# Performance work log

Measured on AMD Instinct MI355X. Metric: run time of the kernel, lower is better.

Reference implementation:

```python
import jax, jax.numpy as jnp
import numpy as np
from jax import lax

EPS = 1e-5
WBITS, BBITS, ABITS = 8, 8, 11  # weight/bias/activation precisions (class defaults)


def _ste_round(x):
    # straight-through estimator round (matches HAWQ-style fake quant)
    return x + lax.stop_gradient(jnp.round(x) - x)


def _quant_weight(w, bits):
    # symmetric per-output-channel weight quantization
    n = 2.0 ** (bits - 1) - 1.0
    s = lax.stop_gradient(jnp.max(jnp.abs(w.reshape(w.shape[0], -1)), axis=1)) / n
    s = jnp.maximum(s, 1e-8)
    w_int = jnp.clip(_ste_round(w / s[:, None, None, None]), -n - 1.0, n)
    return w_int, s


def _conv(x, w, stride, pad):
    return lax.conv_general_dilated(
        x, w, (stride, stride), ((pad, pad), (pad, pad)),
        dimension_numbers=('NCHW', 'OIHW', 'NCHW'))


def _quant_bn_conv(x, act_scale, w, gamma, beta, mean, var, stride, pad):
    # fold BN into conv (QuantBnConv2d), quantize folded weight per channel,
    # integer conv in the x/act_scale domain, rescale back to float
    f = gamma * lax.rsqrt(var + EPS)
    w_f = w * f[:, None, None, None]
    b_f = beta - mean * f
    w_int, w_s = _quant_weight(w_f, WBITS)
    nb = 2.0 ** (BBITS - 1) - 1.0
    b_s = w_s * act_scale  # [O]
    b_int = jnp.clip(_ste_round(b_f / b_s), -nb - 1.0, nb)
    x_int = x / act_scale
    y_int = _conv(x_int, w_int, stride, pad) + b_int[None, :, None, None]
    return y_int * b_s[None, :, None, None], w_s


def _quant_conv(x, act_scale, w, stride, pad):
    # plain QuantConv2d (shortcut path, no bias)
    w_int, w_s = _quant_weight(w, WBITS)
    y_int = _conv(x / act_scale, w_int, stride, pad)
    scale = w_s * act_scale  # [O]
    return y_int * scale[None, :, None, None], w_s


def _quant_act(x, bits):
    # QuantAct: symmetric dynamic requantization to `bits` bits
    n = 2.0 ** (bits - 1) - 1.0
    s = jnp.maximum(lax.stop_gradient(jnp.max(jnp.abs(x))) / n, 1e-8)
    xq = jnp.clip(_ste_round(x / s), -n - 1.0, n) * s
    return xq, s


def setup_inputs() -> dict:
    key = jax.random.key(0)
    ks = jax.random.split(key, 12)
    B, Cin, Cout, H = 64, 128, 256, 56
    return {
        'x': jax.random.normal(ks[0], (B, Cin, H, H), jnp.float32),
        'act_scale': jnp.ones((1,), jnp.float32) * 0.05,
        'w_sc': jax.random.normal(ks[1], (Cout, Cin, 1, 1), jnp.float32) * 0.05,
        'w1': jax.random.normal(ks[2], (Cout, Cin, 3, 3), jnp.float32) * 0.05,
        'g1': jax.random.uniform(ks[3], (Cout,), jnp.float32) + 0.5,
        'b1': jax.random.normal(ks[4], (Cout,), jnp.float32) * 0.1,
        'm1': jax.random.normal(ks[5], (Cout,), jnp.float32) * 0.1,
        'v1': jax.random.uniform(ks[6], (Cout,), jnp.float32) + 0.5,
        'w2': jax.random.normal(ks[7], (Cout, Cout, 3, 3), jnp.float32) * 0.05,
        'g2': jax.random.uniform(ks[8], (Cout,), jnp.float32) + 0.5,
        'b2': jax.random.normal(ks[9], (Cout,), jnp.float32) * 0.1,
        'm2': jax.random.normal(ks[10], (Cout,), jnp.float32) * 0.1,
        'v2': jax.random.uniform(ks[11], (Cout,), jnp.float32) + 0.5,
    }


def reference(x, act_scale, w_sc, w1, g1, b1, m1, v1, w2, g2, b2, m2, v2):
    # resize_identity branch of QBlock.forward (stride-2 stage transition)
    short_x, _ = _quant_conv(x, act_scale, w_sc, stride=2, pad=0)
    out, _ = _quant_bn_conv(x, act_scale, w1, g1, b1, m1, v1, stride=2, pad=1)
    out = jax.nn.relu(out)
    out, a = _quant_act(out, ABITS)
    out, _ = _quant_bn_conv(out, a, w2, g2, b2, m2, v2, stride=1, pad=1)
    out = jax.nn.relu(out)
    out, a = _quant_act(out, ABITS)
    out = jax.nn.relu(out + short_x)
    out, a = _quant_act(out, ABITS)
    return out, a
```

## Files before the change

kernel.cpp:

```cpp
#include <hip/hip_runtime.h>
#include <cstdio>
#include <cstdint>

typedef _Float16 h8 __attribute__((ext_vector_type(8)));
typedef _Float16 h4 __attribute__((ext_vector_type(4)));
typedef _Float16 h2 __attribute__((ext_vector_type(2)));
typedef float f4 __attribute__((ext_vector_type(4)));

#define GLD16(g, l) __builtin_amdgcn_global_load_lds( \
    (const __attribute__((address_space(1))) void*)(g), \
    (__attribute__((address_space(3))) void*)(l), 16, 0, 0)

static constexpr int HOUT = 28;
static constexpr long long NSP = 64LL * HOUT * HOUT;
static constexpr long long NEL = NSP * 256;
static constexpr int NSLOT = 64;
static constexpr int SLOTSTRIDE = 32;

__global__ void init_ws(int* __restrict__ slots, _Float16* __restrict__ zp)
{
    const int t = threadIdx.x;
    for (int i = t; i < 3 * NSLOT * SLOTSTRIDE; i += 256) slots[i] = 0;
    for (int i = t; i < 512; i += 256) zp[i] = (_Float16)0.f;
}

__device__ __forceinline__ float slot_max(const int* __restrict__ slots)
{
    float m = 0.f;
#pragma unroll
    for (int i = 0; i < NSLOT; ++i) m = fmaxf(m, __int_as_float(slots[i * SLOTSTRIDE]));
    return m;
}

__global__ void prep_w1(const float* __restrict__ w1, const float* __restrict__ g1,
                        const float* __restrict__ b1, const float* __restrict__ m1,
                        const float* __restrict__ v1, const float* __restrict__ asp,
                        _Float16* __restrict__ wq, float* __restrict__ scale1,
                        float* __restrict__ bias1)
{
    const int o = blockIdx.x, t = threadIdx.x;
    const float f = g1[o] * rsqrtf(v1[o] + 1e-5f);
    const float* wr = w1 + (size_t)o * 1152;
    float amax = 0.f;
    for (int i = t; i < 1152; i += 256) amax = fmaxf(amax, fabsf(wr[i] * f));
    __shared__ float red[256];
    red[t] = amax; __syncthreads();
    for (int s = 128; s > 0; s >>= 1) { if (t < s) red[t] = fmaxf(red[t], red[t + s]); __syncthreads(); }
    const float ws = fmaxf(red[0] / 127.f, 1e-8f);
    for (int idx = t; idx < 2304; idx += 256) {
        int p = idx >> 8, cc = idx & 255, ci = cc & 127;
        float q = fminf(fmaxf(rintf(wr[ci * 9 + p] * f / ws), -128.f), 127.f);
        wq[(size_t)o * 2304 + idx] = (_Float16)q;
    }
    if (t == 0) {
        const float bs = ws * asp[0];
        const float bf = b1[o] - m1[o] * f;
        float bq = fminf(fmaxf(rintf(bf / bs), -128.f), 127.f);
        scale1[o] = bs;
        bias1[o] = bq * bs;
    }
}

__global__ void prep_w2(const float* __restrict__ w2, const float* __restrict__ g2,
                        const float* __restrict__ b2, const float* __restrict__ m2,
                        const float* __restrict__ v2,
                        _Float16* __restrict__ wq, float* __restrict__ ws2,
                        float* __restrict__ b2f)
{
    const int o = blockIdx.x, t = threadIdx.x;
    const float f = g2[o] * rsqrtf(v2[o] + 1e-5f);
    const float* wr = w2 + (size_t)o * 2304;
    float amax = 0.f;
    for (int i = t; i < 2304; i += 256) amax = fmaxf(amax, fabsf(wr[i] * f));
    __shared__ float red[256];
    red[t] = amax; __syncthreads();
    for (int s = 128; s > 0; s >>= 1) { if (t < s) red[t] = fmaxf(red[t], red[t + s]); __syncthreads(); }
    const float ws = fmaxf(red[0] / 127.f, 1e-8f);
    for (int idx = t; idx < 2304; idx += 256) {
        int p = idx >> 8, ci = idx & 255;
        float q = fminf(fmaxf(rintf(wr[ci * 9 + p] * f / ws), -128.f), 127.f);
        wq[(size_t)o * 2304 + idx] = (_Float16)q;
    }
    if (t == 0) { ws2[o] = ws; b2f[o] = b2[o] - m2[o] * f; }
}

__global__ void prep_wsc(const float* __restrict__ wsc, const float* __restrict__ asp,
                         _Float16* __restrict__ wq, float* __restrict__ scale_sc)
{
    const int o = blockIdx.x, t = threadIdx.x;
    const float* wr = wsc + (size_t)o * 128;
    float amax = (t < 128) ? fabsf(wr[t]) : 0.f;
    __shared__ float red[256];
    red[t] = amax; __syncthreads();
    for (int s = 128; s > 0; s >>= 1) { if (t < s) red[t] = fmaxf(red[t], red[t + s]); __syncthreads(); }
    const float ws = fmaxf(red[0] / 127.f, 1e-8f);
    float q = fminf(fmaxf(rintf(wr[t & 127] / ws), -128.f), 127.f);
    wq[(size_t)o * 256 + t] = (_Float16)q;
    if (t == 0) scale_sc[o] = ws * asp[0];
}

__global__ void prep_x(const float* __restrict__ x, const float* __restrict__ asp,
                       _Float16* __restrict__ xf)
{
    const int b = blockIdx.x / 56, h = blockIdx.x - (blockIdx.x / 56) * 56;
    const float as = asp[0];
    __shared__ float tile[56 * 129];
    const float* src = x + ((size_t)b * 128 * 56 + h) * 56;
    for (int i = threadIdx.x; i < 7168; i += 256) {
        int c = i / 56, ww = i - c * 56;
        tile[ww * 129 + c] = src[(size_t)c * 3136 + ww] / as;
    }
    __syncthreads();
    _Float16* dst = xf + (size_t)(b * 56 + h) * 56 * 256;
    for (int j = threadIdx.x; j < 7168; j += 256) {
        int ww = j >> 7, q = j & 127;
        int cc = q * 2;
        int c0 = cc & 127, c1 = (cc + 1) & 127;
        float x0 = tile[ww * 129 + c0];
        float x1 = tile[ww * 129 + c1];
        h2 o;
        if (cc < 128) { o[0] = (_Float16)x0; o[1] = (_Float16)x1; }
        else {
            _Float16 h0 = (_Float16)x0, h1 = (_Float16)x1;
            o[0] = (_Float16)(x0 - (float)h0);
            o[1] = (_Float16)(x1 - (float)h1);
        }
        *(h2*)&dst[(size_t)j * 2] = o;
    }
}

template<int HINP, int WINP, int STRIDE, bool SC>
__global__ __launch_bounds__(256, 2)
void conv_k(const _Float16* __restrict__ Xf,
            const _Float16* __restrict__ Wq,
            const _Float16* __restrict__ Wsc,
            const float* __restrict__ scale,
            const float* __restrict__ bias,
            const float* __restrict__ scale_sc,
            float* __restrict__ Y,
            float* __restrict__ Ysc,
            int* __restrict__ slots,
            const _Float16* __restrict__ zp)
{
    constexpr int KT = 2304;
    __shared__ __attribute__((aligned(16))) _Float16 As[4096];
    __shared__ __attribute__((aligned(16))) _Float16 Bs[4096];
    __shared__ float wred[4];

    const int t = threadIdx.x;
    const int wave = t >> 6, lane = t & 63;
    const int wm = wave >> 1, wn = wave & 1;
    const int fr = lane & 15, fq = lane >> 4;
    const int m0 = blockIdx.y << 7;
    const int n0 = blockIdx.x << 7;
    const int chunk = t & 3;
    const int rowt = t >> 2;

    int bb[2], oh[2], ow[2];
#pragma unroll
    for (int i = 0; i < 2; ++i) {
        int n = n0 + i * 64 + rowt;
        bb[i] = n / (HOUT * HOUT);
        int r = n - bb[i] * (HOUT * HOUT);
        oh[i] = r / HOUT;
        ow[i] = r - oh[i] * HOUT;
    }

    const char* Ab = (const char*)Wq + ((size_t)m0 * KT + (size_t)chunk * 8) * 2;
    size_t aoff[2];
#pragma unroll
    for (int i = 0; i < 2; ++i) aoff[i] = (size_t)(i * 64 + rowt) * (KT * 2);

    f4 acc[4][4];
    f4 accs[4][4];
#pragma unroll
    for (int i = 0; i < 4; ++i)
#pragma unroll
        for (int j = 0; j < 4; ++j) {
            acc[i][j] = f4{0.f, 0.f, 0.f, 0.f};
            if constexpr (SC) accs[i][j] = f4{0.f, 0.f, 0.f, 0.f};
        }

#pragma unroll 1
    for (int p = 0; p < 9; ++p) {
        const int kh = p / 3, kw = p - kh * 3;
        const char* bsrc[2];
#pragma unroll
        for (int i = 0; i < 2; ++i) {
            int ih = oh[i] * STRIDE - 1 + kh;
            int iw = ow[i] * STRIDE - 1 + kw;
            bool ok = ((unsigned)ih < (unsigned)HINP) && ((unsigned)iw < (unsigned)WINP);
            bsrc[i] = ok ? (const char*)Xf + ((((size_t)bb[i] * HINP + ih) * WINP + iw) * 256 + (size_t)chunk * 8) * 2
                         : (const char*)zp + (size_t)chunk * 16;
        }
        const char* ap = Ab + (size_t)p * 512;
#pragma unroll 1
        for (int kc = 0; kc < 8; ++kc) {
#pragma unroll
            for (int i = 0; i < 2; ++i) {
                GLD16(ap + aoff[i] + kc * 64, (char*)As + i * 4096 + wave * 1024);
                GLD16(bsrc[i] + kc * 64,      (char*)Bs + i * 4096 + wave * 1024);
            }
            __syncthreads();
            h8 af[4], bf[4];
#pragma unroll
            for (int x = 0; x < 4; ++x) {
                af[x] = *(const h8*)&As[(wm * 64 + x * 16 + fr) * 32 + fq * 8];
                bf[x] = *(const h8*)&Bs[(wn * 64 + x * 16 + fr) * 32 + fq * 8];
            }
#pragma unroll
            for (int mi = 0; mi < 4; ++mi)
#pragma unroll
                for (int ni = 0; ni < 4; ++ni)
                    acc[mi][ni] = __builtin_amdgcn_mfma_f32_16x16x32_f16(af[mi], bf[ni], acc[mi][ni], 0, 0, 0);
            if constexpr (SC) {
                if (p == 4) {
                    h8 sf[4];
#pragma unroll
                    for (int mi = 0; mi < 4; ++mi)
                        sf[mi] = *(const h8*)&Wsc[(size_t)(m0 + wm * 64 + mi * 16 + fr) * 256 + kc * 32 + fq * 8];
#pragma unroll
                    for (int mi = 0; mi < 4; ++mi)
#pragma unroll
                        for (int ni = 0; ni < 4; ++ni)
                            accs[mi][ni] = __builtin_amdgcn_mfma_f32_16x16x32_f16(sf[mi], bf[ni], accs[mi][ni], 0, 0, 0);
                }
            }
            __syncthreads();
        }
    }

    float tmax = 0.f;
#pragma unroll
    for (int mi = 0; mi < 4; ++mi) {
        const int m = m0 + wm * 64 + mi * 16 + fq * 4;
        const f4 sc = *(const f4*)&scale[m];
        const f4 bi = *(const f4*)&bias[m];
        f4 ssc;
        if constexpr (SC) ssc = *(const f4*)&scale_sc[m];
#pragma unroll
        for (int ni = 0; ni < 4; ++ni) {
            const int n = n0 + wn * 64 + ni * 16 + fr;
            f4 v = acc[mi][ni] * sc + bi;
            f4 r;
            r.x = fmaxf(v.x, 0.f); r.y = fmaxf(v.y, 0.f);
            r.z = fmaxf(v.z, 0.f); r.w = fmaxf(v.w, 0.f);
            tmax = fmaxf(tmax, fmaxf(fmaxf(r.x, r.y), fmaxf(r.z, r.w)));
            *(f4*)&Y[(size_t)n * 256 + m] = r;
            if constexpr (SC) {
                f4 s = accs[mi][ni] * ssc;
                *(f4*)&Ysc[(size_t)n * 256 + m] = s;
            }
        }
    }
#pragma unroll
    for (int off = 32; off > 0; off >>= 1)
        tmax = fmaxf(tmax, __shfl_xor(tmax, off));
    if (lane == 0) wred[wave] = tmax;
    __syncthreads();
    if (t == 0) {
        float mx = fmaxf(fmaxf(wred[0], wred[1]), fmaxf(wred[2], wred[3]));
        atomicMax(&slots[((blockIdx.x + blockIdx.y * 392) & (NSLOT - 1)) * SLOTSTRIDE],
                  __float_as_int(mx));
    }
}

__global__ void mid_k(const int* __restrict__ slotsA, const float* __restrict__ ws2,
                      const float* __restrict__ b2f, float* __restrict__ scale2,
                      float* __restrict__ bias2, float* __restrict__ a1p)
{
    const int o = threadIdx.x;
    const float a1 = fmaxf(slot_max(slotsA) / 1023.f, 1e-8f);
    const float s2 = ws2[o] * a1;
    float bq = fminf(fmaxf(rintf(b2f[o] / s2), -128.f), 127.f);
    scale2[o] = s2;
    bias2[o] = bq * s2;
    if (o == 0) a1p[0] = a1;
}

__global__ void quant_x2(const float* __restrict__ t1, const float* __restrict__ a1p,
                         _Float16* __restrict__ x2)
{
    const size_t i = (size_t)blockIdx.x * 256 + threadIdx.x;
    const float a1 = a1p[0];
    f4 v = ((const f4*)t1)[i];
    h4 o;
    o[0] = (_Float16)fminf(rintf(v.x / a1), 1023.f);
    o[1] = (_Float16)fminf(rintf(v.y / a1), 1023.f);
    o[2] = (_Float16)fminf(rintf(v.z / a1), 1023.f);
    o[3] = (_Float16)fminf(rintf(v.w / a1), 1023.f);
    ((h4*)x2)[i] = o;
}

__global__ void add_short_k(const float* __restrict__ t2, const float* __restrict__ sh,
                            const int* __restrict__ slotsB, int* __restrict__ slotsC,
                            float* __restrict__ o3)
{
    const float a2 = fmaxf(slot_max(slotsB) / 1023.f, 1e-8f);
    const float inv_a2 = 1.f / a2;
    float tmax = 0.f;
    const size_t base = (size_t)blockIdx.x * 256 + threadIdx.x;
#pragma unroll
    for (int it = 0; it < 4; ++it) {
        const size_t i = base + (size_t)it * 802816;
        f4 v = ((const f4*)t2)[i];
        f4 s = ((const f4*)sh)[i];
        f4 r;
        r.x = fmaxf(fminf(rintf(v.x * inv_a2), 1023.f) * a2 + s.x, 0.f);
        r.y = fmaxf(fminf(rintf(v.y * inv_a2), 1023.f) * a2 + s.y, 0.f);
        r.z = fmaxf(fminf(rintf(v.z * inv_a2), 1023.f) * a2 + s.z, 0.f);
        r.w = fmaxf(fminf(rintf(v.w * inv_a2), 1023.f) * a2 + s.w, 0.f);
        ((f4*)o3)[i] = r;
        tmax = fmaxf(tmax, fmaxf(fmaxf(r.x, r.y), fmaxf(r.z, r.w)));
    }
#pragma unroll
    for (int off = 32; off > 0; off >>= 1)
        tmax = fmaxf(tmax, __shfl_xor(tmax, off));
    __shared__ float wred[4];
    if ((threadIdx.x & 63) == 0) wred[threadIdx.x >> 6] = tmax;
    __syncthreads();
    if (threadIdx.x == 0) {
        float mx = fmaxf(fmaxf(wred[0], wred[1]), fmaxf(wred[2], wred[3]));
        atomicMax(&slotsC[(blockIdx.x & (NSLOT - 1)) * SLOTSTRIDE], __float_as_int(mx));
    }
}

__global__ void finalize_k(const float* __restrict__ o3, const int* __restrict__ slotsC,
                           float* __restrict__ dout, int out_size)
{
    const int b = blockIdx.x / 28, oh = blockIdx.x - (blockIdx.x / 28) * 28;
    const float a3 = fmaxf(slot_max(slotsC) / 1023.f, 1e-8f);
    __shared__ float tile[28 * 257];
    const float* src = o3 + (size_t)(b * 28 + oh) * 28 * 256;
    for (int i = threadIdx.x; i < 7168; i += 256)
        tile[(i >> 8) * 257 + (i & 255)] = src[i];
    __syncthreads();
    for (int j = threadIdx.x; j < 7168; j += 256) {
        int c = j / 28, ww = j - (j / 28) * 28;
        float v = tile[ww * 257 + c];
        float q = fminf(rintf(v / a3), 1023.f);
        dout[(((size_t)b * 256 + c) * 28 + oh) * 28 + ww] = q * a3;
    }
    if (blockIdx.x == 0 && threadIdx.x == 0) dout[(size_t)out_size - 1] = a3;
}

extern "C" void kernel_launch(void* const* d_in, const int* in_sizes, int n_in,
                              void* d_out, int out_size, void* d_ws, size_t ws_size,
                              hipStream_t stream)
{
    const float* x   = (const float*)d_in[0];
    const float* as_ = (const float*)d_in[1];
    const float* wsc = (const float*)d_in[2];
    const float* w1  = (const float*)d_in[3];
    const float* g1  = (const float*)d_in[4];
    const float* b1  = (const float*)d_in[5];
    const float* m1  = (const float*)d_in[6];
    const float* v1  = (const float*)d_in[7];
    const float* w2  = (const float*)d_in[8];
    const float* g2  = (const float*)d_in[9];
    const float* b2  = (const float*)d_in[10];
    const float* m2  = (const float*)d_in[11];
    const float* v2  = (const float*)d_in[12];
    float* out = (float*)d_out;

    char* w = (char*)d_ws;
    size_t off = 0;
    auto alloc = [&](size_t bytes) { size_t c = off; off += (bytes + 255) & ~(size_t)255; return c; };
    const size_t oXF = alloc((size_t)64 * 56 * 56 * 256 * 2);
    const size_t oY1 = alloc((size_t)NEL * 4);
    const size_t oSH = alloc((size_t)NEL * 4);
    const size_t oX2 = alloc((size_t)NEL * 2);
    const size_t oW1 = alloc((size_t)256 * 2304 * 2);
    const size_t oW2 = alloc((size_t)256 * 2304 * 2);
    const size_t oWS = alloc((size_t)256 * 256 * 2);
    const size_t oSC = alloc((size_t)8 * 256 * 4);
    const size_t oMS = alloc(3 * NSLOT * SLOTSTRIDE * 4 + 2048);
    if (off > ws_size) {
        fprintf(stderr, "kernel_launch: ws too small: need %zu have %zu\n", off, ws_size);
        return;
    }

    _Float16* xf   = (_Float16*)(w + oXF);
    float*    y1   = (float*)(w + oY1);
    float*    sh   = (float*)(w + oSH);
    _Float16* x2   = (_Float16*)(w + oX2);
    _Float16* wq1  = (_Float16*)(w + oW1);
    _Float16* wq2  = (_Float16*)(w + oW2);
    _Float16* wscd = (_Float16*)(w + oWS);
    float* scl = (float*)(w + oSC);
    float *scale1 = scl, *bias1 = scl + 256, *scale_sc = scl + 512, *ws2 = scl + 768,
          *b2f = scl + 1024, *scale2 = scl + 1280, *bias2 = scl + 1536, *a1p = scl + 1792;
    int* slots  = (int*)(w + oMS);
    int* slotsA = slots;
    int* slotsB = slots + NSLOT * SLOTSTRIDE;
    int* slotsC = slots + 2 * NSLOT * SLOTSTRIDE;
    _Float16* zp = (_Float16*)(w + oMS + 3 * NSLOT * SLOTSTRIDE * 4);
    float* y2 = (float*)(w + oXF);
    float* o3 = (float*)(w + oY1);

    init_ws<<<1, 256, 0, stream>>>(slots, zp);
    prep_wsc<<<256, 256, 0, stream>>>(wsc, as_, wscd, scale_sc);
    prep_w1<<<256, 256, 0, stream>>>(w1, g1, b1, m1, v1, as_, wq1, scale1, bias1);
    prep_w2<<<256, 256, 0, stream>>>(w2, g2, b2, m2, v2, wq2, ws2, b2f);
    prep_x<<<64 * 56, 256, 0, stream>>>(x, as_, xf);
    conv_k<56, 56, 2, true><<<dim3(392, 2), 256, 0, stream>>>(
        xf, wq1, wscd, scale1, bias1, scale_sc, y1, sh, slotsA, zp);
    mid_k<<<1, 256, 0, stream>>>(slotsA, ws2, b2f, scale2, bias2, a1p);
    quant_x2<<<12544, 256, 0, stream>>>(y1, a1p, x2);
    conv_k<28, 28, 1, false><<<dim3(392, 2), 256, 0, stream>>>(
        x2, wq2, nullptr, scale2, bias2, nullptr, y2, nullptr, slotsB, zp);
    add_short_k<<<3136, 256, 0, stream>>>(y2, sh, slotsB, slotsC, o3);
    finalize_k<<<64 * 28, 256, 0, stream>>>(o3, slotsC, out, out_size);
}
```

Baseline: 362.3 us.

## Double-buffer conv GEMM loads, split shortcut conv, parity-split input layout

Rewrites the implicit-GEMM conv kernel to double-buffer its LDS tiles. The next k-step's global-to-LDS loads are issued before the current MFMAs, using explicit vmcnt waits and raw barriers. The stride-2 input is stored with even and odd columns split apart, giving contiguous gathers, and the shortcut 1x1 conv becomes its own kernel launch instead of being fused into the first conv. The block index is also swizzled and occupancy is raised to 3 blocks per SM. The cost is double the LDS and an extra launch that rereads the input for the shortcut.

```diff
diff --git a/kernel.cpp b/kernel.cpp
--- a/kernel.cpp
+++ b/kernel.cpp
@@ -111,7 +111,7 @@
         tile[ww * 129 + c] = src[(size_t)c * 3136 + ww] / as;
     }
     __syncthreads();
-    _Float16* dst = xf + (size_t)(b * 56 + h) * 56 * 256;
+    _Float16* dst = xf + (size_t)(b * 56 + h) * 2 * 28 * 256;
     for (int j = threadIdx.x; j < 7168; j += 256) {
         int ww = j >> 7, q = j & 127;
         int cc = q * 2;
@@ -125,143 +125,171 @@
             o[0] = (_Float16)(x0 - (float)h0);
             o[1] = (_Float16)(x1 - (float)h1);
         }
-        *(h2*)&dst[(size_t)j * 2] = o;
-    }
-}
-
-template<int HINP, int WINP, int STRIDE, bool SC>
-__global__ __launch_bounds__(256, 2)
+        size_t eo = ((size_t)(ww & 1) * 28 + (ww >> 1)) * 256 + (size_t)cc;
+        *(h2*)&dst[eo] = o;
+    }
+}
+
+template<int MODE>
+__global__ __launch_bounds__(256, 3)
 void conv_k(const _Float16* __restrict__ Xf,
             const _Float16* __restrict__ Wq,
-            const _Float16* __restrict__ Wsc,
             const float* __restrict__ scale,
             const float* __restrict__ bias,
-            const float* __restrict__ scale_sc,
             float* __restrict__ Y,
-            float* __restrict__ Ysc,
             int* __restrict__ slots,
             const _Float16* __restrict__ zp)
 {
-    constexpr int KT = 2304;
-    __shared__ __attribute__((aligned(16))) _Float16 As[4096];
-    __shared__ __attribute__((aligned(16))) _Float16 Bs[4096];
+    constexpr int KT = (MODE == 2) ? 256 : 2304;
+    constexpr int NSTEP = KT / 32;
+    __shared__ __attribute__((aligned(16))) _Float16 As[2][4096];
+    __shared__ __attribute__((aligned(16))) _Float16 Bs[2][4096];
     __shared__ float wred[4];
 
     const int t = threadIdx.x;
     const int wave = t >> 6, lane = t & 63;
     const int wm = wave >> 1, wn = wave & 1;
     const int fr = lane & 15, fq = lane >> 4;
-    const int m0 = blockIdx.y << 7;
-    const int n0 = blockIdx.x << 7;
-    const int chunk = t & 3;
-    const int rowt = t >> 2;
+
+    const int id = blockIdx.x;
+    const int lin = (id & 7) * 98 + (id >> 3);
+    const int m0 = (lin & 1) << 7;
+    const int n0 = (lin >> 1) << 7;
+
+    const int row_d = ((t >> 6) << 4) | (t & 15);
+    const int ch_d  = (t >> 4) & 3;
+
+    const char* aA[2];
+#pragma unroll
+    for (int i = 0; i < 2; ++i)
+        aA[i] = (const char*)Wq + (size_t)(m0 + i * 64 + row_d) * (KT * 2) + ch_d * 16;
 
     int bb[2], oh[2], ow[2];
+    const char* bC[2] = {nullptr, nullptr};
 #pragma unroll
     for (int i = 0; i < 2; ++i) {
-        int n = n0 + i * 64 + rowt;
-        bb[i] = n / (HOUT * HOUT);
-        int r = n - bb[i] * (HOUT * HOUT);
-        oh[i] = r / HOUT;
-        ow[i] = r - oh[i] * HOUT;
-    }
-
-    const char* Ab = (const char*)Wq + ((size_t)m0 * KT + (size_t)chunk * 8) * 2;
-    size_t aoff[2];
-#pragma unroll
-    for (int i = 0; i < 2; ++i) aoff[i] = (size_t)(i * 64 + rowt) * (KT * 2);
+        int n = n0 + i * 64 + row_d;
+        bb[i] = n / 784;
+        int r = n - bb[i] * 784;
+        oh[i] = r / 28;
+        ow[i] = r - oh[i] * 28;
+        if constexpr (MODE == 2)
+            bC[i] = (const char*)Xf +
+                ((((size_t)bb[i] * 56 + oh[i] * 2) * 2 + 0) * 28 + ow[i]) * 512 + ch_d * 16;
+    }
+
+    int aoffr[4], boffr[4];
+#pragma unroll
+    for (int x = 0; x < 4; ++x) {
+        aoffr[x] = wm * 4096 + (x * 64 + fq * 16 + fr) * 16;
+        boffr[x] = wn * 4096 + (x * 64 + fq * 16 + fr) * 16;
+    }
+
+    auto stage = [&](int ks, int buf) {
+        const int kc = ks & 7;
+#pragma unroll
+        for (int i = 0; i < 2; ++i)
+            GLD16(aA[i] + (size_t)ks * 64,
+                  (char*)As + buf * 8192 + i * 4096 + wave * 1024);
+        const int p = ks >> 3;
+        const int kh = p / 3, kw = p - kh * 3;
+#pragma unroll
+        for (int i = 0; i < 2; ++i) {
+            const char* bp;
+            if constexpr (MODE == 2) {
+                bp = bC[i] + ks * 64;
+            } else if constexpr (MODE == 0) {
+                int ih = oh[i] * 2 - 1 + kh;
+                int par = (kw == 1) ? 0 : 1;
+                int j = (kw == 0) ? ow[i] - 1 : ow[i];
+                bool ok = ((unsigned)ih < 56u) && ((unsigned)j < 28u);
+                bp = ok ? (const char*)Xf +
+                          (((((size_t)bb[i] * 56 + ih) * 2 + par) * 28 + j) << 9) + kc * 64 + ch_d * 16
+                        : (const char*)zp + ch_d * 16;
+            } else {
+                int ih = oh[i] - 1 + kh;
+                int iw = ow[i] - 1 + kw;
+                bool ok = ((unsigned)ih < 28u) && ((unsigned)iw < 28u);
+                bp = ok ? (const char*)Xf +
+                          ((((size_t)bb[i] * 28 + ih) * 28 + iw) << 9) + kc * 64 + ch_d * 16
+                        : (const char*)zp + ch_d * 16;
+            }
+            GLD16(bp, (char*)Bs + buf * 8192 + i * 4096 + wave * 1024);
+        }
+    };
 
     f4 acc[4][4];
-    f4 accs[4][4];
 #pragma unroll
     for (int i = 0; i < 4; ++i)
 #pragma unroll
-        for (int j = 0; j < 4; ++j) {
-            acc[i][j] = f4{0.f, 0.f, 0.f, 0.f};
-            if constexpr (SC) accs[i][j] = f4{0.f, 0.f, 0.f, 0.f};
-        }
-
+        for (int j = 0; j < 4; ++j) acc[i][j] = f4{0.f, 0.f, 0.f, 0.f};
+
+    stage(0, 0);
 #pragma unroll 1
-    for (int p = 0; p < 9; ++p) {
-        const int kh = p / 3, kw = p - kh * 3;
-        const char* bsrc[2];
-#pragma unroll
-        for (int i = 0; i < 2; ++i) {
-            int ih = oh[i] * STRIDE - 1 + kh;
-            int iw = ow[i] * STRIDE - 1 + kw;
-            bool ok = ((unsigned)ih < (unsigned)HINP) && ((unsigned)iw < (unsigned)WINP);
-            bsrc[i] = ok ? (const char*)Xf + ((((size_t)bb[i] * HINP + ih) * WINP + iw) * 256 + (size_t)chunk * 8) * 2
-                         : (const char*)zp + (size_t)chunk * 16;
-        }
-        const char* ap = Ab + (size_t)p * 512;
-#pragma unroll 1
-        for (int kc = 0; kc < 8; ++kc) {
-#pragma unroll
-            for (int i = 0; i < 2; ++i) {
-                GLD16(ap + aoff[i] + kc * 64, (char*)As + i * 4096 + wave * 1024);
-                GLD16(bsrc[i] + kc * 64,      (char*)Bs + i * 4096 + wave * 1024);
+    for (int ks = 0; ks < NSTEP; ++ks) {
+        const int cur = ks & 1;
+        if (ks + 1 < NSTEP) {
+            stage(ks + 1, cur ^ 1);
+            asm volatile("s_waitcnt vmcnt(4)" ::: "memory");
+        } else {
+            asm volatile("s_waitcnt vmcnt(0)" ::: "memory");
+        }
+        __builtin_amdgcn_s_barrier();
+        asm volatile("" ::: "memory");
+        h8 af[4], bf[4];
+#pragma unroll
+        for (int x = 0; x < 4; ++x) {
+            af[x] = *(const h8*)((const char*)As + cur * 8192 + aoffr[x]);
+            bf[x] = *(const h8*)((const char*)Bs + cur * 8192 + boffr[x]);
+        }
+#pragma unroll
+        for (int mi = 0; mi < 4; ++mi)
+#pragma unroll
+            for (int ni = 0; ni < 4; ++ni)
+                acc[mi][ni] = __builtin_amdgcn_mfma_f32_16x16x32_f16(af[mi], bf[ni], acc[mi][ni], 0, 0, 0);
+        asm volatile("" ::: "memory");
+        __builtin_amdgcn_s_barrier();
+    }
+
+    if constexpr (MODE == 2) {
+#pragma unroll
+        for (int mi = 0; mi < 4; ++mi) {
+            const int m = m0 + wm * 64 + mi * 16 + fq * 4;
+            const f4 sc = *(const f4*)&scale[m];
+#pragma unroll
+            for (int ni = 0; ni < 4; ++ni) {
+                const int n = n0 + wn * 64 + ni * 16 + fr;
+                f4 s = acc[mi][ni] * sc;
+                *(f4*)&Y[(size_t)n * 256 + m] = s;
             }
-            __syncthreads();
-            h8 af[4], bf[4];
-#pragma unroll
-            for (int x = 0; x < 4; ++x) {
-                af[x] = *(const h8*)&As[(wm * 64 + x * 16 + fr) * 32 + fq * 8];
-                bf[x] = *(const h8*)&Bs[(wn * 64 + x * 16 + fr) * 32 + fq * 8];
+        }
+    } else {
+        float tmax = 0.f;
+#pragma unroll
+        for (int mi = 0; mi < 4; ++mi) {
+            const int m = m0 + wm * 64 + mi * 16 + fq * 4;
+            const f4 sc = *(const f4*)&scale[m];
+            const f4 bi = *(const f4*)&bias[m];
+#pragma unroll
+            for (int ni = 0; ni < 4; ++ni) {
+                const int n = n0 + wn * 64 + ni * 16 + fr;
+                f4 v = acc[mi][ni] * sc + bi;
+                f4 r;
+                r.x = fmaxf(v.x, 0.f); r.y = fmaxf(v.y, 0.f);
+                r.z = fmaxf(v.z, 0.f); r.w = fmaxf(v.w, 0.f);
+                tmax = fmaxf(tmax, fmaxf(fmaxf(r.x, r.y), fmaxf(r.z, r.w)));
+                *(f4*)&Y[(size_t)n * 256 + m] = r;
             }
-#pragma unroll
-            for (int mi = 0; mi < 4; ++mi)
-#pragma unroll
-                for (int ni = 0; ni < 4; ++ni)
-                    acc[mi][ni] = __builtin_amdgcn_mfma_f32_16x16x32_f16(af[mi], bf[ni], acc[mi][ni], 0, 0, 0);
-            if constexpr (SC) {
-                if (p == 4) {
-                    h8 sf[4];
-#pragma unroll
-                    for (int mi = 0; mi < 4; ++mi)
-                        sf[mi] = *(const h8*)&Wsc[(size_t)(m0 + wm * 64 + mi * 16 + fr) * 256 + kc * 32 + fq * 8];
-#pragma unroll
-                    for (int mi = 0; mi < 4; ++mi)
-#pragma unroll
-                        for (int ni = 0; ni < 4; ++ni)
-                            accs[mi][ni] = __builtin_amdgcn_mfma_f32_16x16x32_f16(sf[mi], bf[ni], accs[mi][ni], 0, 0, 0);
-                }
-            }
-            __syncthreads();
-        }
-    }
-
-    float tmax = 0.f;
-#pragma unroll
-    for (int mi = 0; mi < 4; ++mi) {
-        const int m = m0 + wm * 64 + mi * 16 + fq * 4;
-        const f4 sc = *(const f4*)&scale[m];
-        const f4 bi = *(const f4*)&bias[m];
-        f4 ssc;
-        if constexpr (SC) ssc = *(const f4*)&scale_sc[m];
-#pragma unroll
-        for (int ni = 0; ni < 4; ++ni) {
-            const int n = n0 + wn * 64 + ni * 16 + fr;
-            f4 v = acc[mi][ni] * sc + bi;
-            f4 r;
-            r.x = fmaxf(v.x, 0.f); r.y = fmaxf(v.y, 0.f);
-            r.z = fmaxf(v.z, 0.f); r.w = fmaxf(v.w, 0.f);
-            tmax = fmaxf(tmax, fmaxf(fmaxf(r.x, r.y), fmaxf(r.z, r.w)));
-            *(f4*)&Y[(size_t)n * 256 + m] = r;
-            if constexpr (SC) {
-                f4 s = accs[mi][ni] * ssc;
-                *(f4*)&Ysc[(size_t)n * 256 + m] = s;
-            }
-        }
-    }
-#pragma unroll
-    for (int off = 32; off > 0; off >>= 1)
-        tmax = fmaxf(tmax, __shfl_xor(tmax, off));
-    if (lane == 0) wred[wave] = tmax;
-    __syncthreads();
-    if (t == 0) {
-        float mx = fmaxf(fmaxf(wred[0], wred[1]), fmaxf(wred[2], wred[3]));
-        atomicMax(&slots[((blockIdx.x + blockIdx.y * 392) & (NSLOT - 1)) * SLOTSTRIDE],
-                  __float_as_int(mx));
+        }
+#pragma unroll
+        for (int off = 32; off > 0; off >>= 1)
+            tmax = fmaxf(tmax, __shfl_xor(tmax, off));
+        if (lane == 0) wred[wave] = tmax;
+        __syncthreads();
+        if (t == 0) {
+            float mx = fmaxf(fmaxf(wred[0], wred[1]), fmaxf(wred[2], wred[3]));
+            atomicMax(&slots[(lin & (NSLOT - 1)) * SLOTSTRIDE], __float_as_int(mx));
+        }
     }
 }
 
@@ -403,12 +431,11 @@
     prep_w1<<<256, 256, 0, stream>>>(w1, g1, b1, m1, v1, as_, wq1, scale1, bias1);
     prep_w2<<<256, 256, 0, stream>>>(w2, g2, b2, m2, v2, wq2, ws2, b2f);
     prep_x<<<64 * 56, 256, 0, stream>>>(x, as_, xf);
-    conv_k<56, 56, 2, true><<<dim3(392, 2), 256, 0, stream>>>(
-        xf, wq1, wscd, scale1, bias1, scale_sc, y1, sh, slotsA, zp);
+    conv_k<2><<<784, 256, 0, stream>>>(xf, wscd, scale_sc, nullptr, sh, nullptr, zp);
+    conv_k<0><<<784, 256, 0, stream>>>(xf, wq1, scale1, bias1, y1, slotsA, zp);
     mid_k<<<1, 256, 0, stream>>>(slotsA, ws2, b2f, scale2, bias2, a1p);
     quant_x2<<<12544, 256, 0, stream>>>(y1, a1p, x2);
-    conv_k<28, 28, 1, false><<<dim3(392, 2), 256, 0, stream>>>(
-        x2, wq2, nullptr, scale2, bias2, nullptr, y2, nullptr, slotsB, zp);
+    conv_k<1><<<784, 256, 0, stream>>>(x2, wq2, scale2, bias2, y2, slotsB, zp);
     add_short_k<<<3136, 256, 0, stream>>>(y2, sh, slotsB, slotsC, o3);
     finalize_k<<<64 * 28, 256, 0, stream>>>(o3, slotsC, out, out_size);
 }
```

Measured after the change: 455.2 us. 25.6% more time.

## Restructure implicit-GEMM conv with 256x256 tiles and triple-buffered async LDS pipeline

Applied to the files above, without the earlier changes.

The conv kernel now uses 512-thread workgroups, each computing all 256 output channels for 256 spatial positions. It runs a 3-stage global_load_lds ring with vmcnt waits and one barrier per step, replacing the two-barrier single-buffer loop, and raises MFMA priority via setprio. The workgroup-to-XCD mapping is remapped, and prep_x writes x with even/odd width columns split so stride-2 gathers become contiguous. The 1x1 shortcut GEMM moves into a separate epilogue that reads straight from global memory. The aim is to hide load latency and reuse each weight load across more positions, at the cost of one workgroup per CU with a 96KB LDS footprint and only 196 workgroups.

```diff
diff --git a/kernel.cpp b/kernel.cpp
--- a/kernel.cpp
+++ b/kernel.cpp
@@ -111,7 +111,7 @@
         tile[ww * 129 + c] = src[(size_t)c * 3136 + ww] / as;
     }
     __syncthreads();
-    _Float16* dst = xf + (size_t)(b * 56 + h) * 56 * 256;
+    _Float16* dst = xf + (size_t)(b * 56 + h) * 2 * 28 * 256;
     for (int j = threadIdx.x; j < 7168; j += 256) {
         int ww = j >> 7, q = j & 127;
         int cc = q * 2;
@@ -125,12 +125,13 @@
             o[0] = (_Float16)(x0 - (float)h0);
             o[1] = (_Float16)(x1 - (float)h1);
         }
-        *(h2*)&dst[(size_t)j * 2] = o;
-    }
-}
-
-template<int HINP, int WINP, int STRIDE, bool SC>
-__global__ __launch_bounds__(256, 2)
+        size_t eo = ((size_t)(ww & 1) * 28 + (ww >> 1)) * 256 + (size_t)cc;
+        *(h2*)&dst[eo] = o;
+    }
+}
+
+template<int MODE>
+__global__ __launch_bounds__(512, 1)
 void conv_k(const _Float16* __restrict__ Xf,
             const _Float16* __restrict__ Wq,
             const _Float16* __restrict__ Wsc,
@@ -143,101 +144,128 @@
             const _Float16* __restrict__ zp)
 {
     constexpr int KT = 2304;
-    __shared__ __attribute__((aligned(16))) _Float16 As[4096];
-    __shared__ __attribute__((aligned(16))) _Float16 Bs[4096];
-    __shared__ float wred[4];
+    constexpr int NSTEP = 72;
+    __shared__ __attribute__((aligned(16))) _Float16 L[49152];
+    __shared__ float wred[8];
 
     const int t = threadIdx.x;
     const int wave = t >> 6, lane = t & 63;
-    const int wm = wave >> 1, wn = wave & 1;
+    const int wm = wave >> 2;
+    const int wn = wave & 3;
     const int fr = lane & 15, fq = lane >> 4;
-    const int m0 = blockIdx.y << 7;
-    const int n0 = blockIdx.x << 7;
-    const int chunk = t & 3;
-    const int rowt = t >> 2;
-
-    int bb[2], oh[2], ow[2];
-#pragma unroll
-    for (int i = 0; i < 2; ++i) {
-        int n = n0 + i * 64 + rowt;
-        bb[i] = n / (HOUT * HOUT);
-        int r = n - bb[i] * (HOUT * HOUT);
-        oh[i] = r / HOUT;
-        ow[i] = r - oh[i] * HOUT;
-    }
-
-    const char* Ab = (const char*)Wq + ((size_t)m0 * KT + (size_t)chunk * 8) * 2;
-    size_t aoff[2];
-#pragma unroll
-    for (int i = 0; i < 2; ++i) aoff[i] = (size_t)(i * 64 + rowt) * (KT * 2);
-
-    f4 acc[4][4];
-    f4 accs[4][4];
-#pragma unroll
-    for (int i = 0; i < 4; ++i)
-#pragma unroll
-        for (int j = 0; j < 4; ++j) {
-            acc[i][j] = f4{0.f, 0.f, 0.f, 0.f};
-            if constexpr (SC) accs[i][j] = f4{0.f, 0.f, 0.f, 0.f};
-        }
-
+
+    const int orig = blockIdx.x;
+    const int xcd = orig & 7, i8 = orig >> 3;
+    const int wgid = (xcd < 4 ? xcd * 25 : 100 + (xcd - 4) * 24) + i8;
+    const int n0 = wgid << 8;
+
+    const int srow = wn * 64 + lane;
+    const char* aSrc = (const char*)Wq + (size_t)srow * (KT * 2);
+    const int nb = n0 + srow;
+    const int bb = nb / 784;
+    const int rbp = nb - bb * 784;
+    const int ohb = rbp / 28, owb = rbp - (rbp / 28) * 28;
+
+    const char* bptr = (const char*)zp;
+    auto stage = [&](int tt, int slot) {
+        char* base = (char*)L + slot * 32768;
+        if ((tt & 7) == 0) {
+            const int p = tt >> 3;
+            const int kh = p / 3, kw = p - kh * 3;
+            if constexpr (MODE == 0) {
+                int ih = ohb * 2 - 1 + kh;
+                int par = (kw == 1) ? 0 : 1;
+                int j = (kw == 0) ? owb - 1 : owb;
+                bool ok = ((unsigned)ih < 56u) && ((unsigned)j < 28u);
+                bptr = ok ? (const char*)Xf + (((((size_t)bb * 56 + ih) * 2 + par) * 28 + j) << 9)
+                          : (const char*)zp;
+            } else {
+                int ih = ohb - 1 + kh, iw = owb - 1 + kw;
+                bool ok = ((unsigned)ih < 28u) && ((unsigned)iw < 28u);
+                bptr = ok ? (const char*)Xf + ((((size_t)bb * 28 + ih) * 28 + iw) << 9)
+                          : (const char*)zp;
+            }
+        }
+        const size_t ka = (size_t)tt * 64;
+        const int ko = (tt & 7) * 64;
+        GLD16(aSrc + ka + wm * 16,          base + wm * 4096 + wn * 1024);
+        GLD16(aSrc + ka + (2 + wm) * 16,    base + (2 + wm) * 4096 + wn * 1024);
+        GLD16(bptr + ko + wm * 16,          base + 16384 + wm * 4096 + wn * 1024);
+        GLD16(bptr + ko + (2 + wm) * 16,    base + 16384 + (2 + wm) * 4096 + wn * 1024);
+    };
+
+    f4 acc[8][4];
+#pragma unroll
+    for (int i = 0; i < 8; ++i)
+#pragma unroll
+        for (int j = 0; j < 4; ++j) acc[i][j] = f4{0.f, 0.f, 0.f, 0.f};
+
+    stage(0, 0);
+    stage(1, 1);
+    int cs = 0, ns = 2;
 #pragma unroll 1
-    for (int p = 0; p < 9; ++p) {
-        const int kh = p / 3, kw = p - kh * 3;
-        const char* bsrc[2];
-#pragma unroll
-        for (int i = 0; i < 2; ++i) {
-            int ih = oh[i] * STRIDE - 1 + kh;
-            int iw = ow[i] * STRIDE - 1 + kw;
-            bool ok = ((unsigned)ih < (unsigned)HINP) && ((unsigned)iw < (unsigned)WINP);
-            bsrc[i] = ok ? (const char*)Xf + ((((size_t)bb[i] * HINP + ih) * WINP + iw) * 256 + (size_t)chunk * 8) * 2
-                         : (const char*)zp + (size_t)chunk * 16;
-        }
-        const char* ap = Ab + (size_t)p * 512;
-#pragma unroll 1
-        for (int kc = 0; kc < 8; ++kc) {
-#pragma unroll
-            for (int i = 0; i < 2; ++i) {
-                GLD16(ap + aoff[i] + kc * 64, (char*)As + i * 4096 + wave * 1024);
-                GLD16(bsrc[i] + kc * 64,      (char*)Bs + i * 4096 + wave * 1024);
-            }
-            __syncthreads();
-            h8 af[4], bf[4];
-#pragma unroll
-            for (int x = 0; x < 4; ++x) {
-                af[x] = *(const h8*)&As[(wm * 64 + x * 16 + fr) * 32 + fq * 8];
-                bf[x] = *(const h8*)&Bs[(wn * 64 + x * 16 + fr) * 32 + fq * 8];
-            }
-#pragma unroll
-            for (int mi = 0; mi < 4; ++mi)
-#pragma unroll
-                for (int ni = 0; ni < 4; ++ni)
-                    acc[mi][ni] = __builtin_amdgcn_mfma_f32_16x16x32_f16(af[mi], bf[ni], acc[mi][ni], 0, 0, 0);
-            if constexpr (SC) {
-                if (p == 4) {
-                    h8 sf[4];
-#pragma unroll
-                    for (int mi = 0; mi < 4; ++mi)
-                        sf[mi] = *(const h8*)&Wsc[(size_t)(m0 + wm * 64 + mi * 16 + fr) * 256 + kc * 32 + fq * 8];
-#pragma unroll
-                    for (int mi = 0; mi < 4; ++mi)
-#pragma unroll
-                        for (int ni = 0; ni < 4; ++ni)
-                            accs[mi][ni] = __builtin_amdgcn_mfma_f32_16x16x32_f16(sf[mi], bf[ni], accs[mi][ni], 0, 0, 0);
-                }
-            }
-            __syncthreads();
-        }
+    for (int it = 0; it < NSTEP - 1; ++it) {
+        asm volatile("s_waitcnt vmcnt(4)" ::: "memory");
+        __builtin_amdgcn_s_barrier();
+        const _Float16* Sa = &L[cs * 16384];
+        const _Float16* Sb = Sa + 8192;
+        h8 af0[4], af1[4], bf[4];
+#pragma unroll
+        for (int i = 0; i < 4; ++i) {
+            af0[i] = *(const h8*)&Sa[fq * 2048 + (wm * 128 + i * 16 + fr) * 8];
+            bf[i]  = *(const h8*)&Sb[fq * 2048 + (wn * 64 + i * 16 + fr) * 8];
+        }
+#pragma unroll
+        for (int i = 0; i < 4; ++i)
+            af1[i] = *(const h8*)&Sa[fq * 2048 + (wm * 128 + 64 + i * 16 + fr) * 8];
+        if (it + 2 < NSTEP) stage(it + 2, ns);
+        __builtin_amdgcn_s_setprio(1);
+#pragma unroll
+        for (int mi = 0; mi < 4; ++mi)
+#pragma unroll
+            for (int ni = 0; ni < 4; ++ni)
+                acc[mi][ni] = __builtin_amdgcn_mfma_f32_16x16x32_f16(af0[mi], bf[ni], acc[mi][ni], 0, 0, 0);
+#pragma unroll
+        for (int mi = 0; mi < 4; ++mi)
+#pragma unroll
+            for (int ni = 0; ni < 4; ++ni)
+                acc[4 + mi][ni] = __builtin_amdgcn_mfma_f32_16x16x32_f16(af1[mi], bf[ni], acc[4 + mi][ni], 0, 0, 0);
+        __builtin_amdgcn_s_setprio(0);
+        cs = (cs == 2) ? 0 : cs + 1;
+        ns = (ns == 2) ? 0 : ns + 1;
+    }
+    {
+        asm volatile("s_waitcnt vmcnt(0)" ::: "memory");
+        __builtin_amdgcn_s_barrier();
+        const _Float16* Sa = &L[cs * 16384];
+        const _Float16* Sb = Sa + 8192;
+        h8 af0[4], af1[4], bf[4];
+#pragma unroll
+        for (int i = 0; i < 4; ++i) {
+            af0[i] = *(const h8*)&Sa[fq * 2048 + (wm * 128 + i * 16 + fr) * 8];
+            bf[i]  = *(const h8*)&Sb[fq * 2048 + (wn * 64 + i * 16 + fr) * 8];
+        }
+#pragma unroll
+        for (int i = 0; i < 4; ++i)
+            af1[i] = *(const h8*)&Sa[fq * 2048 + (wm * 128 + 64 + i * 16 + fr) * 8];
+#pragma unroll
+        for (int mi = 0; mi < 4; ++mi)
+#pragma unroll
+            for (int ni = 0; ni < 4; ++ni)
+                acc[mi][ni] = __builtin_amdgcn_mfma_f32_16x16x32_f16(af0[mi], bf[ni], acc[mi][ni], 0, 0, 0);
+#pragma unroll
+        for (int mi = 0; mi < 4; ++mi)
+#pragma unroll
+            for (int ni = 0; ni < 4; ++ni)
+                acc[4 + mi][ni] = __builtin_amdgcn_mfma_f32_16x16x32_f16(af1[mi], bf[ni], acc[4 + mi][ni], 0, 0, 0);
     }
 
     float tmax = 0.f;
 #pragma unroll
-    for (int mi = 0; mi < 4; ++mi) {
-        const int m = m0 + wm * 64 + mi * 16 + fq * 4;
+    for (int mi = 0; mi < 8; ++mi) {
+        const int m = wm * 128 + mi * 16 + fq * 4;
         const f4 sc = *(const f4*)&scale[m];
         const f4 bi = *(const f4*)&bias[m];
-        f4 ssc;
-        if constexpr (SC) ssc = *(const f4*)&scale_sc[m];
 #pragma unroll
         for (int ni = 0; ni < 4; ++ni) {
             const int n = n0 + wn * 64 + ni * 16 + fr;
@@ -247,10 +275,6 @@
             r.z = fmaxf(v.z, 0.f); r.w = fmaxf(v.w, 0.f);
             tmax = fmaxf(tmax, fmaxf(fmaxf(r.x, r.y), fmaxf(r.z, r.w)));
             *(f4*)&Y[(size_t)n * 256 + m] = r;
-            if constexpr (SC) {
-                f4 s = accs[mi][ni] * ssc;
-                *(f4*)&Ysc[(size_t)n * 256 + m] = s;
-            }
         }
     }
 #pragma unroll
@@ -259,9 +283,53 @@
     if (lane == 0) wred[wave] = tmax;
     __syncthreads();
     if (t == 0) {
-        float mx = fmaxf(fmaxf(wred[0], wred[1]), fmaxf(wred[2], wred[3]));
-        atomicMax(&slots[((blockIdx.x + blockIdx.y * 392) & (NSLOT - 1)) * SLOTSTRIDE],
-                  __float_as_int(mx));
+        float mx = 0.f;
+#pragma unroll
+        for (int i = 0; i < 8; ++i) mx = fmaxf(mx, wred[i]);
+        atomicMax(&slots[(wgid & (NSLOT - 1)) * SLOTSTRIDE], __float_as_int(mx));
+    }
+
+    if constexpr (MODE == 0) {
+        const char* pb[4];
+#pragma unroll
+        for (int ni = 0; ni < 4; ++ni) {
+            int n = n0 + wn * 64 + ni * 16 + fr;
+            int b2 = n / 784;
+            int r2 = n - b2 * 784;
+            int oh2 = r2 / 28, ow2 = r2 - (r2 / 28) * 28;
+            pb[ni] = (const char*)Xf + (((((size_t)b2 * 56 + oh2 * 2) * 2 + 0) * 28 + ow2) << 9);
+        }
+#pragma unroll
+        for (int i = 0; i < 8; ++i)
+#pragma unroll
+            for (int j = 0; j < 4; ++j) acc[i][j] = f4{0.f, 0.f, 0.f, 0.f};
+#pragma unroll 1
+        for (int st = 0; st < 8; ++st) {
+            h8 sf[8], bg[4];
+#pragma unroll
+            for (int mi = 0; mi < 8; ++mi)
+                sf[mi] = *(const h8*)((const char*)Wsc +
+                         (size_t)(wm * 128 + mi * 16 + fr) * 512 + st * 64 + fq * 16);
+#pragma unroll
+            for (int ni = 0; ni < 4; ++ni)
+                bg[ni] = *(const h8*)(pb[ni] + st * 64 + fq * 16);
+#pragma unroll
+            for (int mi = 0; mi < 8; ++mi)
+#pragma unroll
+                for (int ni = 0; ni < 4; ++ni)
+                    acc[mi][ni] = __builtin_amdgcn_mfma_f32_16x16x32_f16(sf[mi], bg[ni], acc[mi][ni], 0, 0, 0);
+        }
+#pragma unroll
+        for (int mi = 0; mi < 8; ++mi) {
+            const int m = wm * 128 + mi * 16 + fq * 4;
+            const f4 ssc = *(const f4*)&scale_sc[m];
+#pragma unroll
+            for (int ni = 0; ni < 4; ++ni) {
+                const int n = n0 + wn * 64 + ni * 16 + fr;
+                f4 s = acc[mi][ni] * ssc;
+                *(f4*)&Ysc[(size_t)n * 256 + m] = s;
+            }
+        }
     }
 }
 
@@ -403,12 +471,12 @@
     prep_w1<<<256, 256, 0, stream>>>(w1, g1, b1, m1, v1, as_, wq1, scale1, bias1);
     prep_w2<<<256, 256, 0, stream>>>(w2, g2, b2, m2, v2, wq2, ws2, b2f);
     prep_x<<<64 * 56, 256, 0, stream>>>(x, as_, xf);
-    conv_k<56, 56, 2, true><<<dim3(392, 2), 256, 0, stream>>>(
-        xf, wq1, wscd, scale1, bias1, scale_sc, y1, sh, slotsA, zp);
+    conv_k<0><<<196, 512, 0, stream>>>(xf, wq1, wscd, scale1, bias1, scale_sc,
+                                       y1, sh, slotsA, zp);
     mid_k<<<1, 256, 0, stream>>>(slotsA, ws2, b2f, scale2, bias2, a1p);
     quant_x2<<<12544, 256, 0, stream>>>(y1, a1p, x2);
-    conv_k<28, 28, 1, false><<<dim3(392, 2), 256, 0, stream>>>(
-        x2, wq2, nullptr, scale2, bias2, nullptr, y2, nullptr, slotsB, zp);
+    conv_k<1><<<196, 512, 0, stream>>>(x2, wq2, nullptr, scale2, bias2, nullptr,
+                                       y2, nullptr, slotsB, zp);
     add_short_k<<<3136, 256, 0, stream>>>(y2, sh, slotsB, slotsC, o3);
     finalize_k<<<64 * 28, 256, 0, stream>>>(o3, slotsC, out, out_size);
 }
```

New measurement: 366.4 us. No clear change (+1.1%).

## Move shortcut GEMM to conv epilogue, raise occupancy, fuse add into finalize

Applied to the files above, without the earlier changes.

The 1x1 shortcut conv no longer runs interleaved in the main K loop with a second 64-register accumulator set. It now runs after the main epilogue, reusing the same accumulators and reading operands directly from global memory. This frees registers so launch bounds can ask for 3 blocks per CU. The add-shortcut kernel now only computes the max, and finalize recomputes the add and requant from y2 and sh. That drops the o3 write and read but makes finalize read two arrays.

```diff
diff --git a/kernel.cpp b/kernel.cpp
--- a/kernel.cpp
+++ b/kernel.cpp
@@ -130,7 +130,7 @@
 }
 
 template<int HINP, int WINP, int STRIDE, bool SC>
-__global__ __launch_bounds__(256, 2)
+__global__ __launch_bounds__(256, 3)
 void conv_k(const _Float16* __restrict__ Xf,
             const _Float16* __restrict__ Wq,
             const _Float16* __restrict__ Wsc,
@@ -172,14 +172,10 @@
     for (int i = 0; i < 2; ++i) aoff[i] = (size_t)(i * 64 + rowt) * (KT * 2);
 
     f4 acc[4][4];
-    f4 accs[4][4];
 #pragma unroll
     for (int i = 0; i < 4; ++i)
 #pragma unroll
-        for (int j = 0; j < 4; ++j) {
-            acc[i][j] = f4{0.f, 0.f, 0.f, 0.f};
-            if constexpr (SC) accs[i][j] = f4{0.f, 0.f, 0.f, 0.f};
-        }
+        for (int j = 0; j < 4; ++j) acc[i][j] = f4{0.f, 0.f, 0.f, 0.f};
 
 #pragma unroll 1
     for (int p = 0; p < 9; ++p) {
@@ -213,19 +209,6 @@
 #pragma unroll
                 for (int ni = 0; ni < 4; ++ni)
                     acc[mi][ni] = __builtin_amdgcn_mfma_f32_16x16x32_f16(af[mi], bf[ni], acc[mi][ni], 0, 0, 0);
-            if constexpr (SC) {
-                if (p == 4) {
-                    h8 sf[4];
-#pragma unroll
-                    for (int mi = 0; mi < 4; ++mi)
-                        sf[mi] = *(const h8*)&Wsc[(size_t)(m0 + wm * 64 + mi * 16 + fr) * 256 + kc * 32 + fq * 8];
-#pragma unroll
-                    for (int mi = 0; mi < 4; ++mi)
-#pragma unroll
-                        for (int ni = 0; ni < 4; ++ni)
-                            accs[mi][ni] = __builtin_amdgcn_mfma_f32_16x16x32_f16(sf[mi], bf[ni], accs[mi][ni], 0, 0, 0);
-                }
-            }
             __syncthreads();
         }
     }
@@ -236,8 +219,6 @@
         const int m = m0 + wm * 64 + mi * 16 + fq * 4;
         const f4 sc = *(const f4*)&scale[m];
         const f4 bi = *(const f4*)&bias[m];
-        f4 ssc;
-        if constexpr (SC) ssc = *(const f4*)&scale_sc[m];
 #pragma unroll
         for (int ni = 0; ni < 4; ++ni) {
             const int n = n0 + wn * 64 + ni * 16 + fr;
@@ -247,10 +228,6 @@
             r.z = fmaxf(v.z, 0.f); r.w = fmaxf(v.w, 0.f);
             tmax = fmaxf(tmax, fmaxf(fmaxf(r.x, r.y), fmaxf(r.z, r.w)));
             *(f4*)&Y[(size_t)n * 256 + m] = r;
-            if constexpr (SC) {
-                f4 s = accs[mi][ni] * ssc;
-                *(f4*)&Ysc[(size_t)n * 256 + m] = s;
-            }
         }
     }
 #pragma unroll
@@ -262,6 +239,49 @@
         float mx = fmaxf(fmaxf(wred[0], wred[1]), fmaxf(wred[2], wred[3]));
         atomicMax(&slots[((blockIdx.x + blockIdx.y * 392) & (NSLOT - 1)) * SLOTSTRIDE],
                   __float_as_int(mx));
+    }
+
+    if constexpr (SC) {
+        const char* pb[4];
+#pragma unroll
+        for (int ni = 0; ni < 4; ++ni) {
+            int n = n0 + wn * 64 + ni * 16 + fr;
+            int b2 = n / 784;
+            int r2 = n - b2 * 784;
+            int oh2 = r2 / 28, ow2 = r2 - (r2 / 28) * 28;
+            pb[ni] = (const char*)Xf + (((size_t)b2 * 56 + oh2 * 2) * 56 + ow2 * 2) * 512;
+        }
+#pragma unroll
+        for (int i = 0; i < 4; ++i)
+#pragma unroll
+            for (int j = 0; j < 4; ++j) acc[i][j] = f4{0.f, 0.f, 0.f, 0.f};
+#pragma unroll
+        for (int st = 0; st < 8; ++st) {
+            h8 sf[4], bg[4];
+#pragma unroll
+            for (int mi = 0; mi < 4; ++mi)
+                sf[mi] = *(const h8*)((const char*)Wsc +
+                         (size_t)(m0 + wm * 64 + mi * 16 + fr) * 512 + st * 64 + fq * 16);
+#pragma unroll
+            for (int ni = 0; ni < 4; ++ni)
+                bg[ni] = *(const h8*)(pb[ni] + st * 64 + fq * 16);
+#pragma unroll
+            for (int mi = 0; mi < 4; ++mi)
+#pragma unroll
+                for (int ni = 0; ni < 4; ++ni)
+                    acc[mi][ni] = __builtin_amdgcn_mfma_f32_16x16x32_f16(sf[mi], bg[ni], acc[mi][ni], 0, 0, 0);
+        }
+#pragma unroll
+        for (int mi = 0; mi < 4; ++mi) {
+            const int m = m0 + wm * 64 + mi * 16 + fq * 4;
+            const f4 ssc = *(const f4*)&scale_sc[m];
+#pragma unroll
+            for (int ni = 0; ni < 4; ++ni) {
+                const int n = n0 + wn * 64 + ni * 16 + fr;
+                f4 s = acc[mi][ni] * ssc;
+                *(f4*)&Ysc[(size_t)n * 256 + m] = s;
+            }
+        }
     }
 }
 
@@ -292,9 +312,8 @@
     ((h4*)x2)[i] = o;
 }
 
-__global__ void add_short_k(const float* __restrict__ t2, const float* __restrict__ sh,
-                            const int* __restrict__ slotsB, int* __restrict__ slotsC,
-                            float* __restrict__ o3)
+__global__ void max_k(const float* __restrict__ t2, const float* __restrict__ sh,
+                      const int* __restrict__ slotsB, int* __restrict__ slotsC)
 {
     const float a2 = fmaxf(slot_max(slotsB) / 1023.f, 1e-8f);
     const float inv_a2 = 1.f / a2;
@@ -310,7 +329,6 @@
         r.y = fmaxf(fminf(rintf(v.y * inv_a2), 1023.f) * a2 + s.y, 0.f);
         r.z = fmaxf(fminf(rintf(v.z * inv_a2), 1023.f) * a2 + s.z, 0.f);
         r.w = fmaxf(fminf(rintf(v.w * inv_a2), 1023.f) * a2 + s.w, 0.f);
-        ((f4*)o3)[i] = r;
         tmax = fmaxf(tmax, fmaxf(fmaxf(r.x, r.y), fmaxf(r.z, r.w)));
     }
 #pragma unroll
@@ -325,15 +343,22 @@
     }
 }
 
-__global__ void finalize_k(const float* __restrict__ o3, const int* __restrict__ slotsC,
+__global__ void finalize_k(const float* __restrict__ t2, const float* __restrict__ sh,
+                           const int* __restrict__ slotsB, const int* __restrict__ slotsC,
                            float* __restrict__ dout, int out_size)
 {
     const int b = blockIdx.x / 28, oh = blockIdx.x - (blockIdx.x / 28) * 28;
+    const float a2 = fmaxf(slot_max(slotsB) / 1023.f, 1e-8f);
+    const float inv_a2 = 1.f / a2;
     const float a3 = fmaxf(slot_max(slotsC) / 1023.f, 1e-8f);
     __shared__ float tile[28 * 257];
-    const float* src = o3 + (size_t)(b * 28 + oh) * 28 * 256;
-    for (int i = threadIdx.x; i < 7168; i += 256)
-        tile[(i >> 8) * 257 + (i & 255)] = src[i];
+    const size_t rowbase = (size_t)(b * 28 + oh) * 28 * 256;
+    for (int i = threadIdx.x; i < 7168; i += 256) {
+        float v = t2[rowbase + i];
+        float s = sh[rowbase + i];
+        float r = fmaxf(fminf(rintf(v * inv_a2), 1023.f) * a2 + s, 0.f);
+        tile[(i >> 8) * 257 + (i & 255)] = r;
+    }
     __syncthreads();
     for (int j = threadIdx.x; j < 7168; j += 256) {
         int c = j / 28, ww = j - (j / 28) * 28;
@@ -396,7 +421,6 @@
     int* slotsC = slots + 2 * NSLOT * SLOTSTRIDE;
     _Float16* zp = (_Float16*)(w + oMS + 3 * NSLOT * SLOTSTRIDE * 4);
     float* y2 = (float*)(w + oXF);
-    float* o3 = (float*)(w + oY1);
 
     init_ws<<<1, 256, 0, stream>>>(slots, zp);
     prep_wsc<<<256, 256, 0, stream>>>(wsc, as_, wscd, scale_sc);
@@ -409,6 +433,6 @@
     quant_x2<<<12544, 256, 0, stream>>>(y1, a1p, x2);
     conv_k<28, 28, 1, false><<<dim3(392, 2), 256, 0, stream>>>(
         x2, wq2, nullptr, scale2, bias2, nullptr, y2, nullptr, slotsB, zp);
-    add_short_k<<<3136, 256, 0, stream>>>(y2, sh, slotsB, slotsC, o3);
-    finalize_k<<<64 * 28, 256, 0, stream>>>(o3, slotsC, out, out_size);
-}
+    max_k<<<3136, 256, 0, stream>>>(y2, sh, slotsB, slotsC);
+    finalize_k<<<64 * 28, 256, 0, stream>>>(y2, sh, slotsB, slotsC, out, out_size);
+}
```

New measurement: 376.4 us. 1.04x slower.
